# Optimization experiments

Hardware: AMD Instinct MI355X
Metric: run time of the kernel (lower is better)

Reference implementation:

```python
import math
import jax, jax.numpy as jnp
import numpy as np

B, S, D = 8, 1024, 1024
H, DK = 16, 64
NUM_BUCKETS, MAX_DIST = 32, 128


def _relative_position_bucket(relative_position, num_buckets=NUM_BUCKETS, max_distance=MAX_DIST):
    # bidirectional=True branch of T5's bucket fn
    nb = num_buckets // 2
    n = -relative_position
    ret = (n < 0).astype(jnp.int32) * nb
    n = jnp.abs(n)
    max_exact = nb // 2
    is_small = n < max_exact
    n_safe = jnp.maximum(n, 1).astype(jnp.float32)
    val_if_large = max_exact + (
        jnp.log(n_safe / max_exact) / math.log(max_distance / max_exact) * (nb - max_exact)
    ).astype(jnp.int32)
    val_if_large = jnp.minimum(val_if_large, nb - 1)
    return ret + jnp.where(is_small, n, val_if_large)


def compute_bias(rel_emb, qlen, klen):
    ctx = jnp.arange(qlen)[:, None]
    mem = jnp.arange(klen)[None, :]
    rp_bucket = _relative_position_bucket(mem - ctx)          # [q, k]
    values = rel_emb[rp_bucket]                                # [q, k, H]
    return jnp.transpose(values, (2, 0, 1))[None]              # [1, H, q, k]


def setup_inputs() -> dict:
    key = jax.random.key(0)
    ks = jax.random.split(key, 6)
    sc = 0.02
    return {
        "x": jax.random.normal(ks[0], (B, S, D), jnp.float32),
        "Wq": jax.random.normal(ks[1], (D, H * DK), jnp.float32) * sc,
        "Wk": jax.random.normal(ks[2], (D, H * DK), jnp.float32) * sc,
        "Wv": jax.random.normal(ks[3], (D, H * DK), jnp.float32) * sc,
        "Wo": jax.random.normal(ks[4], (H * DK, D), jnp.float32) * sc,
        "rel_emb": jax.random.normal(ks[5], (NUM_BUCKETS, H), jnp.float32),
    }


def reference(x, Wq, Wk, Wv, Wo, rel_emb):
    bs, qlen, _ = x.shape

    def shape(t):  # [B, S, H*DK] -> [B, H, S, DK]
        return t.reshape(bs, -1, H, DK).transpose(0, 2, 1, 3)

    q = shape(x @ Wq)
    k = shape(x @ Wk)
    v = shape(x @ Wv)
    # T5 attention: NO 1/sqrt(dk) scaling
    scores = jnp.einsum("bhqd,bhkd->bhqk", q, k)
    position_bias = compute_bias(rel_emb, qlen, qlen)
    scores = scores + position_bias
    weights = jax.nn.softmax(scores.astype(jnp.float32), axis=-1).astype(scores.dtype)
    context = jnp.einsum("bhqk,bhkd->bhqd", weights, v)
    context = context.transpose(0, 2, 1, 3).reshape(bs, qlen, H * DK)
    return context @ Wo
```

## Files before the change

### kernel.cpp

```cpp
#include <hip/hip_runtime.h>
#include <stdint.h>

typedef uint16_t u16;
typedef uint32_t u32;
typedef __bf16 bf16;
typedef bf16 bf16x8 __attribute__((ext_vector_type(8)));
typedef bf16 bf16x4 __attribute__((ext_vector_type(4)));
typedef float f32x4 __attribute__((ext_vector_type(4)));
typedef u16 u16x4 __attribute__((ext_vector_type(4)));

#define MFMA(a, b, c) __builtin_amdgcn_mfma_f32_16x16x32_bf16((a), (b), (c), 0, 0, 0)

#define BATCH 8
#define SEQ 1024
#define DMODEL 1024
#define NH 16
#define DK 64
#define LOG2E 1.4426950408889634f

__device__ __forceinline__ u16 bfbits(float f) {
    bf16 h = (bf16)f;
    return __builtin_bit_cast(u16, h);
}

__device__ __forceinline__ float exp2_raw(float x) {
    float r;
    asm("v_exp_f32 %0, %1" : "=v"(r) : "v"(x));
    return r;
}

__device__ __forceinline__ void gload_lds16(const u16* g, u16* l) {
    __builtin_amdgcn_global_load_lds(
        (__attribute__((address_space(1))) void*)g,
        (__attribute__((address_space(3))) void*)l, 16, 0, 0);
}

__global__ __launch_bounds__(256) void convert_x_kernel(const float* __restrict__ x,
                                                        u16* __restrict__ xb) {
    size_t id = (size_t)blockIdx.x * 256 + threadIdx.x;
    f32x4 v = *(const f32x4*)(x + id * 4);
    bf16x4 o;
    o[0] = (bf16)v[0]; o[1] = (bf16)v[1]; o[2] = (bf16)v[2]; o[3] = (bf16)v[3];
    *(bf16x4*)(xb + id * 4) = o;
}

__global__ __launch_bounds__(256) void convert_wt_kernel(
        const float* __restrict__ W0, const float* __restrict__ W1,
        const float* __restrict__ W2, const float* __restrict__ W3,
        u16* __restrict__ T0, u16* __restrict__ T1,
        u16* __restrict__ T2, u16* __restrict__ T3) {
    __shared__ u16 Ts[64 * 72];
    const int z = blockIdx.z;
    const float* W = (z == 0) ? W0 : (z == 1) ? W1 : (z == 2) ? W2 : W3;
    u16* T = (z == 0) ? T0 : (z == 1) ? T1 : (z == 2) ? T2 : T3;
    const int k0 = blockIdx.y * 64, n0 = blockIdx.x * 64;
    const int tid = threadIdx.x;
    const int r16 = tid >> 4, c0 = (tid & 15) * 4;
    #pragma unroll
    for (int rr = 0; rr < 4; rr++) {
        int r = rr * 16 + r16;
        f32x4 vv = *(const f32x4*)&W[(size_t)(k0 + r) * 1024 + n0 + c0];
        #pragma unroll
        for (int i = 0; i < 4; i++) Ts[(c0 + i) * 72 + r] = bfbits(vv[i]);
    }
    __syncthreads();
    int n = tid >> 2, seg = (tid & 3) * 16;
    *(bf16x8*)&T[(size_t)(n0 + n) * 1024 + k0 + seg] = *(const bf16x8*)&Ts[n * 72 + seg];
    *(bf16x8*)&T[(size_t)(n0 + n) * 1024 + k0 + seg + 8] =
        *(const bf16x8*)&Ts[n * 72 + seg + 8];
}

__global__ __launch_bounds__(256) void bias_f4_kernel(const float* __restrict__ rel_emb,
                                                      f32x4* __restrict__ F4) {
    int id = blockIdx.x * 256 + threadIdx.x;
    if (id >= NH * 2047) return;
    int h = id / 2047, t = id % 2047;
    f32x4 o;
    #pragma unroll
    for (int j = 0; j < 4; j++) {
        int tt = t + j;
        float val = 0.f;
        if (tt <= 2046) {
            int rel = tt - 1023;
            int n = -rel;
            int b = 0;
            if (n < 0) { b = 16; n = -n; }
            int v;
            if (n < 8) {
                v = n;
            } else {
                int e = 31 - __clz(n);
                int f = 2 * e + ((unsigned)(n * n) >= (1u << (2 * e + 1)) ? 1 : 0);
                v = min(2 + f, 15);
            }
            val = LOG2E * rel_emb[(b + v) * NH + h];
        }
        o[j] = val;
    }
    F4[(size_t)h * 2047 + t] = o;
}

__global__ __launch_bounds__(256) void gemm_qkv_kernel(
        const u16* __restrict__ xb,
        const u16* __restrict__ Wqt, const u16* __restrict__ Wkt, const u16* __restrict__ Wvt,
        u16* __restrict__ qb, u16* __restrict__ kb, u16* __restrict__ vb) {
    __shared__ u16 As[128 * 32];
    __shared__ u16 Bs[128 * 32];
    const int z = blockIdx.y >> 3;
    const u16* Bt = (z == 0) ? Wqt : (z == 1) ? Wkt : Wvt;
    const int m0 = blockIdx.x * 128, n0 = (blockIdx.y & 7) * 128;
    const int tid = threadIdx.x, w = tid >> 6, lane = tid & 63;
    const int quad = lane >> 4, l16 = lane & 15;
    const int rw = w >> 1, cw = w & 1;
    const int srow = lane >> 2, sseg = lane & 3;

    f32x4 acc[4][4];
    #pragma unroll
    for (int i = 0; i < 4; i++)
        #pragma unroll
        for (int j = 0; j < 4; j++) acc[i][j] = (f32x4){0.f, 0.f, 0.f, 0.f};

    for (int kk = 0; kk < 1024; kk += 32) {
        __syncthreads();
        #pragma unroll
        for (int r = 0; r < 2; r++) {
            int base = r * 64 + w * 16;
            int row = base + srow;
            gload_lds16(&xb[(size_t)(m0 + row) * 1024 + kk + sseg * 8], &As[base * 32]);
            gload_lds16(&Bt[(size_t)(n0 + row) * 1024 + kk + sseg * 8], &Bs[base * 32]);
        }
        __syncthreads();
        bf16x8 af[4], bfr[4];
        #pragma unroll
        for (int mt = 0; mt < 4; mt++)
            af[mt] = *(const bf16x8*)&As[(rw * 64 + mt * 16 + l16) * 32 + quad * 8];
        #pragma unroll
        for (int nt = 0; nt < 4; nt++)
            bfr[nt] = *(const bf16x8*)&Bs[(cw * 64 + nt * 16 + l16) * 32 + quad * 8];
        #pragma unroll
        for (int mt = 0; mt < 4; mt++)
            #pragma unroll
            for (int nt = 0; nt < 4; nt++)
                acc[mt][nt] = MFMA(af[mt], bfr[nt], acc[mt][nt]);
    }

    #pragma unroll
    for (int mt = 0; mt < 4; mt++) {
        int gmBase = m0 + rw * 64 + mt * 16 + quad * 4;
        #pragma unroll
        for (int nt = 0; nt < 4; nt++) {
            int gn = n0 + cw * 64 + nt * 16 + l16;
            int h = gn >> 6, dk = gn & 63;
            if (z == 2) {
                int b_ = gmBase >> 10, s0 = gmBase & 1023;
                u16x4 pk = { bfbits(acc[mt][nt][0]), bfbits(acc[mt][nt][1]),
                             bfbits(acc[mt][nt][2]), bfbits(acc[mt][nt][3]) };
                *(u16x4*)&vb[(((size_t)b_ * NH + h) * DK + dk) * SEQ + s0] = pk;
            } else {
                u16* o = z ? kb : qb;
                #pragma unroll
                for (int r = 0; r < 4; r++) {
                    int gm = gmBase + r;
                    int b_ = gm >> 10, s = gm & 1023;
                    float sv = acc[mt][nt][r];
                    if (z == 0) sv *= LOG2E;
                    o[(((size_t)b_ * NH + h) * SEQ + s) * DK + dk] = bfbits(sv);
                }
            }
        }
    }
}

__global__ __launch_bounds__(256) void gemm_out_kernel(
        const u16* __restrict__ ctx, const u16* __restrict__ Wot, float* __restrict__ out) {
    __shared__ u16 As[128 * 32];
    __shared__ u16 Bs[128 * 32];
    const int m0 = blockIdx.x * 128, n0 = blockIdx.y * 128;
    const int tid = threadIdx.x, w = tid >> 6, lane = tid & 63;
    const int quad = lane >> 4, l16 = lane & 15;
    const int rw = w >> 1, cw = w & 1;
    const int srow = lane >> 2, sseg = lane & 3;

    f32x4 acc[4][4];
    #pragma unroll
    for (int i = 0; i < 4; i++)
        #pragma unroll
        for (int j = 0; j < 4; j++) acc[i][j] = (f32x4){0.f, 0.f, 0.f, 0.f};

    for (int kk = 0; kk < 1024; kk += 32) {
        __syncthreads();
        #pragma unroll
        for (int r = 0; r < 2; r++) {
            int base = r * 64 + w * 16;
            int row = base + srow;
            gload_lds16(&ctx[(size_t)(m0 + row) * 1024 + kk + sseg * 8], &As[base * 32]);
            gload_lds16(&Wot[(size_t)(n0 + row) * 1024 + kk + sseg * 8], &Bs[base * 32]);
        }
        __syncthreads();
        bf16x8 af[4], bfr[4];
        #pragma unroll
        for (int mt = 0; mt < 4; mt++)
            af[mt] = *(const bf16x8*)&As[(rw * 64 + mt * 16 + l16) * 32 + quad * 8];
        #pragma unroll
        for (int nt = 0; nt < 4; nt++)
            bfr[nt] = *(const bf16x8*)&Bs[(cw * 64 + nt * 16 + l16) * 32 + quad * 8];
        #pragma unroll
        for (int mt = 0; mt < 4; mt++)
            #pragma unroll
            for (int nt = 0; nt < 4; nt++)
                acc[mt][nt] = MFMA(af[mt], bfr[nt], acc[mt][nt]);
    }

    #pragma unroll
    for (int mt = 0; mt < 4; mt++) {
        int gmBase = m0 + rw * 64 + mt * 16 + quad * 4;
        #pragma unroll
        for (int nt = 0; nt < 4; nt++) {
            int gn = n0 + cw * 64 + nt * 16 + l16;
            #pragma unroll
            for (int r = 0; r < 4; r++)
                out[(size_t)(gmBase + r) * 1024 + gn] = acc[mt][nt][r];
        }
    }
}

__global__ __launch_bounds__(256) void attn_kernel(
        const u16* __restrict__ qb, const u16* __restrict__ kb,
        const u16* __restrict__ vb, const f32x4* __restrict__ F4,
        u16* __restrict__ ctx) {
    __shared__ u16 Kt[64 * 72];
    __shared__ u16 Vt[64 * 72];
    __shared__ u16 Pt[4][32 * 40];
    const int bh = blockIdx.x;
    const int h = bh & (NH - 1), b_ = bh >> 4;
    const int tid = threadIdx.x, w = tid >> 6, lane = tid & 63;
    const int quad = lane >> 4, l16 = lane & 15;
    const int q0 = blockIdx.y * 128 + w * 32;

    const f32x4* F4h = F4 + (size_t)h * 2047;

    bf16x8 bq[2][2];
    #pragma unroll
    for (int mt = 0; mt < 2; mt++) {
        const u16* qrow = qb + ((size_t)bh * SEQ + q0 + mt * 16 + l16) * DK;
        bq[mt][0] = *(const bf16x8*)(qrow + quad * 8);
        bq[mt][1] = *(const bf16x8*)(qrow + 32 + quad * 8);
    }

    float l_[2] = {0.f, 0.f};
    f32x4 oacc[2][4];
    #pragma unroll
    for (int mt = 0; mt < 2; mt++)
        #pragma unroll
        for (int dt = 0; dt < 4; dt++) oacc[mt][dt] = (f32x4){0.f, 0.f, 0.f, 0.f};

    const int srow = tid >> 3, sseg = tid & 7;

    const u16* kbase_p = kb + (size_t)bh * SEQ * DK;
    const u16* vbase_p = vb + (size_t)bh * DK * SEQ;

    bf16x8 kr0 = *(const bf16x8*)&kbase_p[(size_t)srow * DK + sseg * 8];
    bf16x8 kr1 = *(const bf16x8*)&kbase_p[(size_t)(srow + 32) * DK + sseg * 8];
    bf16x8 vr0 = *(const bf16x8*)&vbase_p[(size_t)srow * SEQ + sseg * 8];
    bf16x8 vr1 = *(const bf16x8*)&vbase_p[(size_t)(srow + 32) * SEQ + sseg * 8];

    for (int kt = 0; kt < 16; kt++) {
        const int kbase = kt * 64;
        __syncthreads();
        *(bf16x8*)&Kt[srow * 72 + sseg * 8] = kr0;
        *(bf16x8*)&Kt[(srow + 32) * 72 + sseg * 8] = kr1;
        *(bf16x8*)&Vt[srow * 72 + sseg * 8] = vr0;
        *(bf16x8*)&Vt[(srow + 32) * 72 + sseg * 8] = vr1;
        if (kt < 15) {
            const int nb = kbase + 64;
            kr0 = *(const bf16x8*)&kbase_p[(size_t)(nb + srow) * DK + sseg * 8];
            kr1 = *(const bf16x8*)&kbase_p[(size_t)(nb + srow + 32) * DK + sseg * 8];
            vr0 = *(const bf16x8*)&vbase_p[(size_t)srow * SEQ + nb + sseg * 8];
            vr1 = *(const bf16x8*)&vbase_p[(size_t)(srow + 32) * SEQ + nb + sseg * 8];
        }
        __syncthreads();

        f32x4 sc[2][4];
        #pragma unroll
        for (int mt = 0; mt < 2; mt++)
            #pragma unroll
            for (int nt = 0; nt < 4; nt++) {
                int t0 = (kbase + nt * 16 + quad * 4) - (q0 + mt * 16 + l16) + 1023;
                sc[mt][nt] = F4h[t0];
            }
        #pragma unroll
        for (int nt = 0; nt < 4; nt++) {
            bf16x8 ak0 = *(const bf16x8*)&Kt[(nt * 16 + l16) * 72 + quad * 8];
            bf16x8 ak1 = *(const bf16x8*)&Kt[(nt * 16 + l16) * 72 + 32 + quad * 8];
            #pragma unroll
            for (int mt = 0; mt < 2; mt++) {
                sc[mt][nt] = MFMA(ak0, bq[mt][0], sc[mt][nt]);
                sc[mt][nt] = MFMA(ak1, bq[mt][1], sc[mt][nt]);
            }
        }

        #pragma unroll
        for (int c = 0; c < 2; c++) {
            #pragma unroll
            for (int mt = 0; mt < 2; mt++) {
                #pragma unroll
                for (int i = 0; i < 2; i++) {
                    int nt = 2 * c + i;
                    float p0 = exp2_raw(sc[mt][nt][0]);
                    float p1 = exp2_raw(sc[mt][nt][1]);
                    float p2 = exp2_raw(sc[mt][nt][2]);
                    float p3 = exp2_raw(sc[mt][nt][3]);
                    l_[mt] += (p0 + p1) + (p2 + p3);
                    bf16x4 pk;
                    pk[0] = (bf16)p0; pk[1] = (bf16)p1;
                    pk[2] = (bf16)p2; pk[3] = (bf16)p3;
                    *(bf16x4*)&Pt[w][(mt * 16 + l16) * 40 + i * 16 + quad * 4] = pk;
                }
            }
            bf16x8 bp[2];
            #pragma unroll
            for (int mt = 0; mt < 2; mt++)
                bp[mt] = *(const bf16x8*)&Pt[w][(mt * 16 + l16) * 40 + quad * 8];
            #pragma unroll
            for (int dt = 0; dt < 4; dt++) {
                bf16x8 av = *(const bf16x8*)&Vt[(dt * 16 + l16) * 72 + c * 32 + quad * 8];
                #pragma unroll
                for (int mt = 0; mt < 2; mt++)
                    oacc[mt][dt] = MFMA(av, bp[mt], oacc[mt][dt]);
            }
        }
    }

    #pragma unroll
    for (int mt = 0; mt < 2; mt++) {
        float l = l_[mt];
        l += __shfl_xor(l, 16, 64);
        l += __shfl_xor(l, 32, 64);
        float inv = 1.f / l;
        int gq = q0 + mt * 16 + l16;
        #pragma unroll
        for (int dt = 0; dt < 4; dt++) {
            u16x4 pk = { bfbits(oacc[mt][dt][0] * inv), bfbits(oacc[mt][dt][1] * inv),
                         bfbits(oacc[mt][dt][2] * inv), bfbits(oacc[mt][dt][3] * inv) };
            *(u16x4*)&ctx[((size_t)b_ * SEQ + gq) * DMODEL + h * DK + dt * 16 + quad * 4] = pk;
        }
    }
}

extern "C" void kernel_launch(void* const* d_in, const int* in_sizes, int n_in,
                              void* d_out, int out_size, void* d_ws, size_t ws_size,
                              hipStream_t stream) {
    const float* x   = (const float*)d_in[0];
    const float* Wq  = (const float*)d_in[1];
    const float* Wk  = (const float*)d_in[2];
    const float* Wv  = (const float*)d_in[3];
    const float* Wo  = (const float*)d_in[4];
    const float* rel = (const float*)d_in[5];
    float* out = (float*)d_out;

    char* p = (char*)d_ws;
    u16* xb  = (u16*)p; p += (size_t)BATCH * SEQ * DMODEL * 2;
    u16* Wqt = (u16*)p; p += (size_t)DMODEL * DMODEL * 2;
    u16* Wkt = (u16*)p; p += (size_t)DMODEL * DMODEL * 2;
    u16* Wvt = (u16*)p; p += (size_t)DMODEL * DMODEL * 2;
    u16* Wot = (u16*)p; p += (size_t)DMODEL * DMODEL * 2;
    u16* qb  = (u16*)p; p += (size_t)BATCH * NH * SEQ * DK * 2;
    u16* kb  = (u16*)p; p += (size_t)BATCH * NH * SEQ * DK * 2;
    u16* vb  = (u16*)p; p += (size_t)BATCH * NH * SEQ * DK * 2;
    u16* ctx = (u16*)p; p += (size_t)BATCH * SEQ * DMODEL * 2;
    f32x4* F4 = (f32x4*)p; p += (size_t)NH * 2047 * 16;

    convert_x_kernel<<<8192, 256, 0, stream>>>(x, xb);
    convert_wt_kernel<<<dim3(16, 16, 4), 256, 0, stream>>>(Wq, Wk, Wv, Wo, Wqt, Wkt, Wvt, Wot);
    bias_f4_kernel<<<128, 256, 0, stream>>>(rel, F4);

    gemm_qkv_kernel<<<dim3(64, 24), 256, 0, stream>>>(xb, Wqt, Wkt, Wvt, qb, kb, vb);

    attn_kernel<<<dim3(128, 8), 256, 0, stream>>>(qb, kb, vb, F4, ctx);

    gemm_out_kernel<<<dim3(64, 8), 256, 0, stream>>>(ctx, Wot, out);
}
```

Measured before the change: 253.6 us.

## Merge prep kernels into one launch and double attention query tile per wave

```diff
diff --git a/kernel.cpp b/kernel.cpp
--- a/kernel.cpp
+++ b/kernel.cpp
@@ -35,69 +35,67 @@
         (__attribute__((address_space(3))) void*)l, 16, 0, 0);
 }
 
-__global__ __launch_bounds__(256) void convert_x_kernel(const float* __restrict__ x,
-                                                        u16* __restrict__ xb) {
-    size_t id = (size_t)blockIdx.x * 256 + threadIdx.x;
-    f32x4 v = *(const f32x4*)(x + id * 4);
-    bf16x4 o;
-    o[0] = (bf16)v[0]; o[1] = (bf16)v[1]; o[2] = (bf16)v[2]; o[3] = (bf16)v[3];
-    *(bf16x4*)(xb + id * 4) = o;
-}
-
-__global__ __launch_bounds__(256) void convert_wt_kernel(
-        const float* __restrict__ W0, const float* __restrict__ W1,
-        const float* __restrict__ W2, const float* __restrict__ W3,
-        u16* __restrict__ T0, u16* __restrict__ T1,
-        u16* __restrict__ T2, u16* __restrict__ T3) {
+__global__ __launch_bounds__(256) void prep_kernel(
+        const float* __restrict__ x, const float* __restrict__ W0,
+        const float* __restrict__ W1, const float* __restrict__ W2,
+        const float* __restrict__ W3, const float* __restrict__ rel_emb,
+        u16* __restrict__ xb, u16* __restrict__ T0, u16* __restrict__ T1,
+        u16* __restrict__ T2, u16* __restrict__ T3, f32x4* __restrict__ F4) {
     __shared__ u16 Ts[64 * 72];
-    const int z = blockIdx.z;
-    const float* W = (z == 0) ? W0 : (z == 1) ? W1 : (z == 2) ? W2 : W3;
-    u16* T = (z == 0) ? T0 : (z == 1) ? T1 : (z == 2) ? T2 : T3;
-    const int k0 = blockIdx.y * 64, n0 = blockIdx.x * 64;
-    const int tid = threadIdx.x;
-    const int r16 = tid >> 4, c0 = (tid & 15) * 4;
-    #pragma unroll
-    for (int rr = 0; rr < 4; rr++) {
-        int r = rr * 16 + r16;
-        f32x4 vv = *(const f32x4*)&W[(size_t)(k0 + r) * 1024 + n0 + c0];
-        #pragma unroll
-        for (int i = 0; i < 4; i++) Ts[(c0 + i) * 72 + r] = bfbits(vv[i]);
-    }
-    __syncthreads();
-    int n = tid >> 2, seg = (tid & 3) * 16;
-    *(bf16x8*)&T[(size_t)(n0 + n) * 1024 + k0 + seg] = *(const bf16x8*)&Ts[n * 72 + seg];
-    *(bf16x8*)&T[(size_t)(n0 + n) * 1024 + k0 + seg + 8] =
-        *(const bf16x8*)&Ts[n * 72 + seg + 8];
-}
-
-__global__ __launch_bounds__(256) void bias_f4_kernel(const float* __restrict__ rel_emb,
-                                                      f32x4* __restrict__ F4) {
-    int id = blockIdx.x * 256 + threadIdx.x;
-    if (id >= NH * 2047) return;
-    int h = id / 2047, t = id % 2047;
-    f32x4 o;
-    #pragma unroll
-    for (int j = 0; j < 4; j++) {
-        int tt = t + j;
-        float val = 0.f;
-        if (tt <= 2046) {
-            int rel = tt - 1023;
-            int n = -rel;
-            int b = 0;
-            if (n < 0) { b = 16; n = -n; }
-            int v;
-            if (n < 8) {
-                v = n;
-            } else {
-                int e = 31 - __clz(n);
-                int f = 2 * e + ((unsigned)(n * n) >= (1u << (2 * e + 1)) ? 1 : 0);
-                v = min(2 + f, 15);
-            }
-            val = LOG2E * rel_emb[(b + v) * NH + h];
-        }
-        o[j] = val;
-    }
-    F4[(size_t)h * 2047 + t] = o;
+    const int bid = blockIdx.x, tid = threadIdx.x;
+    if (bid < 8192) {
+        size_t id = (size_t)bid * 256 + tid;
+        f32x4 v = *(const f32x4*)(x + id * 4);
+        bf16x4 o;
+        o[0] = (bf16)v[0]; o[1] = (bf16)v[1]; o[2] = (bf16)v[2]; o[3] = (bf16)v[3];
+        *(bf16x4*)(xb + id * 4) = o;
+    } else if (bid < 9216) {
+        const int t = bid - 8192;
+        const int z = t >> 8, rem = t & 255;
+        const float* W = (z == 0) ? W0 : (z == 1) ? W1 : (z == 2) ? W2 : W3;
+        u16* T = (z == 0) ? T0 : (z == 1) ? T1 : (z == 2) ? T2 : T3;
+        const int k0 = (rem >> 4) * 64, n0 = (rem & 15) * 64;
+        const int r16 = tid >> 4, c0 = (tid & 15) * 4;
+        #pragma unroll
+        for (int rr = 0; rr < 4; rr++) {
+            int r = rr * 16 + r16;
+            f32x4 vv = *(const f32x4*)&W[(size_t)(k0 + r) * 1024 + n0 + c0];
+            #pragma unroll
+            for (int i = 0; i < 4; i++) Ts[(c0 + i) * 72 + r] = bfbits(vv[i]);
+        }
+        __syncthreads();
+        int n = tid >> 2, seg = (tid & 3) * 16;
+        *(bf16x8*)&T[(size_t)(n0 + n) * 1024 + k0 + seg] = *(const bf16x8*)&Ts[n * 72 + seg];
+        *(bf16x8*)&T[(size_t)(n0 + n) * 1024 + k0 + seg + 8] =
+            *(const bf16x8*)&Ts[n * 72 + seg + 8];
+    } else {
+        int id = (bid - 9216) * 256 + tid;
+        if (id >= NH * 2047) return;
+        int h = id / 2047, tt0 = id % 2047;
+        f32x4 o;
+        #pragma unroll
+        for (int j = 0; j < 4; j++) {
+            int tt = tt0 + j;
+            float val = 0.f;
+            if (tt <= 2046) {
+                int rel = tt - 1023;
+                int n = -rel;
+                int b = 0;
+                if (n < 0) { b = 16; n = -n; }
+                int v;
+                if (n < 8) {
+                    v = n;
+                } else {
+                    int e = 31 - __clz(n);
+                    int f = 2 * e + ((unsigned)(n * n) >= (1u << (2 * e + 1)) ? 1 : 0);
+                    v = min(2 + f, 15);
+                }
+                val = LOG2E * rel_emb[(b + v) * NH + h];
+            }
+            o[j] = val;
+        }
+        F4[(size_t)h * 2047 + tt0] = o;
+    }
 }
 
 __global__ __launch_bounds__(256) void gemm_qkv_kernel(
@@ -230,27 +228,27 @@
         u16* __restrict__ ctx) {
     __shared__ u16 Kt[64 * 72];
     __shared__ u16 Vt[64 * 72];
-    __shared__ u16 Pt[4][32 * 40];
+    __shared__ u16 Pt[4][64 * 40];
     const int bh = blockIdx.x;
     const int h = bh & (NH - 1), b_ = bh >> 4;
     const int tid = threadIdx.x, w = tid >> 6, lane = tid & 63;
     const int quad = lane >> 4, l16 = lane & 15;
-    const int q0 = blockIdx.y * 128 + w * 32;
+    const int q0 = blockIdx.y * 256 + w * 64;
 
     const f32x4* F4h = F4 + (size_t)h * 2047;
 
-    bf16x8 bq[2][2];
-    #pragma unroll
-    for (int mt = 0; mt < 2; mt++) {
+    bf16x8 bq[4][2];
+    #pragma unroll
+    for (int mt = 0; mt < 4; mt++) {
         const u16* qrow = qb + ((size_t)bh * SEQ + q0 + mt * 16 + l16) * DK;
         bq[mt][0] = *(const bf16x8*)(qrow + quad * 8);
         bq[mt][1] = *(const bf16x8*)(qrow + 32 + quad * 8);
     }
 
-    float l_[2] = {0.f, 0.f};
-    f32x4 oacc[2][4];
-    #pragma unroll
-    for (int mt = 0; mt < 2; mt++)
+    float l_[4] = {0.f, 0.f, 0.f, 0.f};
+    f32x4 oacc[4][4];
+    #pragma unroll
+    for (int mt = 0; mt < 4; mt++)
         #pragma unroll
         for (int dt = 0; dt < 4; dt++) oacc[mt][dt] = (f32x4){0.f, 0.f, 0.f, 0.f};
 
@@ -280,9 +278,9 @@
         }
         __syncthreads();
 
-        f32x4 sc[2][4];
-        #pragma unroll
-        for (int mt = 0; mt < 2; mt++)
+        f32x4 sc[4][4];
+        #pragma unroll
+        for (int mt = 0; mt < 4; mt++)
             #pragma unroll
             for (int nt = 0; nt < 4; nt++) {
                 int t0 = (kbase + nt * 16 + quad * 4) - (q0 + mt * 16 + l16) + 1023;
@@ -293,7 +291,7 @@
             bf16x8 ak0 = *(const bf16x8*)&Kt[(nt * 16 + l16) * 72 + quad * 8];
             bf16x8 ak1 = *(const bf16x8*)&Kt[(nt * 16 + l16) * 72 + 32 + quad * 8];
             #pragma unroll
-            for (int mt = 0; mt < 2; mt++) {
+            for (int mt = 0; mt < 4; mt++) {
                 sc[mt][nt] = MFMA(ak0, bq[mt][0], sc[mt][nt]);
                 sc[mt][nt] = MFMA(ak1, bq[mt][1], sc[mt][nt]);
             }
@@ -302,7 +300,7 @@
         #pragma unroll
         for (int c = 0; c < 2; c++) {
             #pragma unroll
-            for (int mt = 0; mt < 2; mt++) {
+            for (int mt = 0; mt < 4; mt++) {
                 #pragma unroll
                 for (int i = 0; i < 2; i++) {
                     int nt = 2 * c + i;
@@ -317,22 +315,22 @@
                     *(bf16x4*)&Pt[w][(mt * 16 + l16) * 40 + i * 16 + quad * 4] = pk;
                 }
             }
-            bf16x8 bp[2];
-            #pragma unroll
-            for (int mt = 0; mt < 2; mt++)
+            bf16x8 bp[4];
+            #pragma unroll
+            for (int mt = 0; mt < 4; mt++)
                 bp[mt] = *(const bf16x8*)&Pt[w][(mt * 16 + l16) * 40 + quad * 8];
             #pragma unroll
             for (int dt = 0; dt < 4; dt++) {
                 bf16x8 av = *(const bf16x8*)&Vt[(dt * 16 + l16) * 72 + c * 32 + quad * 8];
                 #pragma unroll
-                for (int mt = 0; mt < 2; mt++)
+                for (int mt = 0; mt < 4; mt++)
                     oacc[mt][dt] = MFMA(av, bp[mt], oacc[mt][dt]);
             }
         }
     }
 
     #pragma unroll
-    for (int mt = 0; mt < 2; mt++) {
+    for (int mt = 0; mt < 4; mt++) {
         float l = l_[mt];
         l += __shfl_xor(l, 16, 64);
         l += __shfl_xor(l, 32, 64);
@@ -370,13 +368,12 @@
     u16* ctx = (u16*)p; p += (size_t)BATCH * SEQ * DMODEL * 2;
     f32x4* F4 = (f32x4*)p; p += (size_t)NH * 2047 * 16;
 
-    convert_x_kernel<<<8192, 256, 0, stream>>>(x, xb);
-    convert_wt_kernel<<<dim3(16, 16, 4), 256, 0, stream>>>(Wq, Wk, Wv, Wo, Wqt, Wkt, Wvt, Wot);
-    bias_f4_kernel<<<128, 256, 0, stream>>>(rel, F4);
+    prep_kernel<<<9344, 256, 0, stream>>>(x, Wq, Wk, Wv, Wo, rel,
+                                          xb, Wqt, Wkt, Wvt, Wot, F4);
 
     gemm_qkv_kernel<<<dim3(64, 24), 256, 0, stream>>>(xb, Wqt, Wkt, Wvt, qb, kb, vb);
 
-    attn_kernel<<<dim3(128, 8), 256, 0, stream>>>(qb, kb, vb, F4, ctx);
+    attn_kernel<<<dim3(128, 4), 256, 0, stream>>>(qb, kb, vb, F4, ctx);
 
     gemm_out_kernel<<<dim3(64, 8), 256, 0, stream>>>(ctx, Wot, out);
 }
```

After: 258.9 us. +2.1%, slower.
